# Performance work log

Measured on AMD Instinct MI355X. Metric: run time of the kernel, lower is better.

## Reference

```python
import jax, jax.numpy as jnp
import numpy as np

B, F, N = 16, 64, 32768
C0, C1, C2 = 64, 16, 1
TOP_K = 64
EPS = 1e-5


def setup_inputs() -> dict:
    key = jax.random.key(0)
    ks = jax.random.split(key, 6)
    def rn(k, shape, scale=1.0):
        return jax.random.normal(k, shape, dtype=jnp.float32) * scale
    return {
        "sortvec": rn(ks[0], (B, 1, F, N)),
        "input": rn(ks[1], (B, F, N)),
        # conv0: kernel (F,1), in=1, out=64 -> weight reduces to [C0, F]
        "w0": rn(ks[2], (C0, F), np.sqrt(2.0 / F)), "b0": jnp.zeros((C0,), jnp.float32),
        "w1": rn(ks[3], (C1, C0), np.sqrt(2.0 / C0)), "b1": jnp.zeros((C1,), jnp.float32),
        "w2": rn(ks[4], (C2, C1), np.sqrt(2.0 / C1)), "b2": jnp.zeros((C2,), jnp.float32),
        "g0": jnp.ones((C0,), jnp.float32), "bt0": jnp.zeros((C0,), jnp.float32),
        "g1": jnp.ones((C1,), jnp.float32), "bt1": jnp.zeros((C1,), jnp.float32),
        "g2": jnp.ones((C2,), jnp.float32), "bt2": jnp.zeros((C2,), jnp.float32),
    }


def _bn_relu(x, g, b):
    # training-mode BatchNorm2d over (B, N) per channel; x: [B, C, N]
    mu = jnp.mean(x, axis=(0, 2), keepdims=True)
    var = jnp.var(x, axis=(0, 2), keepdims=True)
    return jax.nn.relu((x - mu) * jax.lax.rsqrt(var + EPS) * g[None, :, None] + b[None, :, None])


def reference(sortvec, input, w0, b0, w1, b1, w2, b2, g0, bt0, g1, bt1, g2, bt2):
    # conv0 with kernel (F,1) collapses the feature axis: [B,1,F,N] -> [B,C0,N]
    x = jnp.einsum('bfn,of->bon', sortvec[:, 0], w0) + b0[None, :, None]
    x = _bn_relu(x, g0, bt0)
    x = _bn_relu(jnp.einsum('bcn,oc->bon', x, w1) + b1[None, :, None], g1, bt1)
    score = _bn_relu(jnp.einsum('bcn,oc->bon', x, w2) + b2[None, :, None], g2, bt2)  # [B,1,N]
    _, idx = jax.lax.top_k(score[:, 0], TOP_K)                                        # [B,K]
    sorted_input = jnp.take_along_axis(input, idx[:, None, :], axis=2)                # [B,F,K]
    sorted_score = jnp.take_along_axis(score, idx[:, None, :], axis=2)                # [B,1,K]
    feat = jnp.concatenate([sorted_input, sorted_score], axis=1)                      # [B,F+1,K]
    return feat, idx
```

## Files before the change

kernel.cpp:

```cpp
#include <hip/hip_runtime.h>


constexpr int   B_   = 16;
constexpr int   N_   = 32768;
constexpr int   K_   = 64;
constexpr long long S_ = (long long)B_ * N_;
constexpr float EPS_ = 1e-5f;

constexpr int NB0   = 2048;
constexpr int NB1   = 2048;
constexpr int NB2   = 256;
constexpr int NBINS = 4096;
constexpr int CAP   = 1024;

__device__ __forceinline__ unsigned key_map(float f) {
  unsigned u = __float_as_uint(f);
  return (u & 0x80000000u) ? ~u : (u | 0x80000000u);
}

__device__ __forceinline__ void gload16(const float* g, float* l) {
  __builtin_amdgcn_global_load_lds(
      (const __attribute__((address_space(1))) void*)g,
      (__attribute__((address_space(3))) void*)l, 16, 0, 0);
}

__device__ __forceinline__ void stage_tile(const float* __restrict__ src,
                                           float (*dst)[64], int t) {
#pragma unroll
  for (int q = 0; q < 4; ++q) {
    const int e = t + q * 256;
    const int f = e >> 4, c4 = (e & 15) << 2;
    gload16(src + (long long)f * N_ + c4, &dst[f][c4]);
  }
}

__global__ __launch_bounds__(256) void k_prep(const float* __restrict__ w0,
                                              const float* __restrict__ w1,
                                              float* __restrict__ w0T,
                                              float* __restrict__ w1p) {
  int t = threadIdx.x;
  for (int e = t; e < 64 * 64; e += 256) {
    int o = e >> 6, f = e & 63;
    w0T[f * 64 + o] = w0[e];
  }
  for (int e = t; e < 16 * 64; e += 256) {
    int cg = e >> 8, rem = e & 255, o = rem >> 4, j = rem & 15;
    w1p[e] = w1[o * 64 + cg * 16 + j];
  }
}

__global__ __launch_bounds__(256) void k_stat0(const float* __restrict__ sv,
                                               const float* __restrict__ w0T,
                                               const float* __restrict__ b0,
                                               float* __restrict__ p0,
                                               int* __restrict__ ghist) {
  __shared__ float svt[2][64][64];
  const int t   = threadIdx.x;
  const int p   = t & 63;
  const int cg  = __builtin_amdgcn_readfirstlane(t >> 6);
  const int bid = blockIdx.x;

  if (t < 32) ghist[bid * 32 + t] = 0;

  float bb[16];
#pragma unroll
  for (int j = 0; j < 16; ++j) bb[j] = b0[cg * 16 + j];

  float s1[16], s2[16];
#pragma unroll
  for (int j = 0; j < 16; ++j) { s1[j] = 0.f; s2[j] = 0.f; }

  {
    const int tile = bid;
    const int b = tile >> 9, n0 = (tile & 511) << 6;
    stage_tile(sv + ((long long)b * 64) * N_ + n0, svt[0], t);
  }
  int cur = 0;
#pragma unroll
  for (int i = 0; i < 4; ++i) {
    __syncthreads();
    if (i + 1 < 4) {
      const int tile = bid + (i + 1) * NB0;
      const int b = tile >> 9, n0 = (tile & 511) << 6;
      stage_tile(sv + ((long long)b * 64) * N_ + n0, svt[cur ^ 1], t);
    }
    float y[16];
#pragma unroll
    for (int j = 0; j < 16; ++j) y[j] = bb[j];
    for (int f = 0; f < 64; ++f) {
      const float x = svt[cur][f][p];
      const float* wr = w0T + f * 64 + cg * 16;
#pragma unroll
      for (int j = 0; j < 16; ++j) y[j] = fmaf(wr[j], x, y[j]);
    }
#pragma unroll
    for (int j = 0; j < 16; ++j) {
      s1[j] += y[j];
      s2[j] = fmaf(y[j], y[j], s2[j]);
    }
    cur ^= 1;
  }

#pragma unroll
  for (int j = 0; j < 16; ++j) {
#pragma unroll
    for (int off = 32; off; off >>= 1) {
      s1[j] += __shfl_down(s1[j], off, 64);
      s2[j] += __shfl_down(s2[j], off, 64);
    }
  }
  if (p == 0) {
    float* dst = p0 + (long long)bid * 128;
#pragma unroll
    for (int j = 0; j < 16; ++j) {
      dst[cg * 16 + j]      = s1[j];
      dst[64 + cg * 16 + j] = s2[j];
    }
  }
}

__global__ __launch_bounds__(1024) void k_reduce0(const float* __restrict__ p0,
                                                  const float* __restrict__ g,
                                                  const float* __restrict__ bt,
                                                  float* __restrict__ st) {
  __shared__ float l[8][128];
  const int t = threadIdx.x;
  const int j = t & 127, grp = t >> 7;
  float a = 0.f;
  for (int i = grp; i < NB0; i += 8) a += p0[(long long)i * 128 + j];
  l[grp][j] = a;
  __syncthreads();
  if (t < 128) {
    float v = ((l[0][t] + l[1][t]) + (l[2][t] + l[3][t])) +
              ((l[4][t] + l[5][t]) + (l[6][t] + l[7][t]));
    l[0][t] = v;
  }
  __syncthreads();
  if (t < 64) {
    const float inv = 1.f / (float)S_;
    float mean = l[0][t] * inv;
    float ex2  = l[0][64 + t] * inv;
    float var  = ex2 - mean * mean;
    float sc   = g[t] * rsqrtf(var + EPS_);
    st[t]      = sc;
    st[64 + t] = bt[t] - mean * sc;
  }
}

__global__ __launch_bounds__(256) void k_layer01(const float* __restrict__ sv,
                                                 const float* __restrict__ w0T,
                                                 const float* __restrict__ b0,
                                                 const float* __restrict__ st0,
                                                 const float* __restrict__ w1p,
                                                 const float* __restrict__ b1,
                                                 float* __restrict__ y1,
                                                 float* __restrict__ p1) {
  __shared__ float svt[2][64][64];
  __shared__ float zp[4][16][64];
  const int t   = threadIdx.x;
  const int p   = t & 63;
  const int cg  = __builtin_amdgcn_readfirstlane(t >> 6);
  const int bid = blockIdx.x;

  float bb[16], sc[16], sh[16];
#pragma unroll
  for (int j = 0; j < 16; ++j) {
    bb[j] = b0[cg * 16 + j];
    sc[j] = st0[cg * 16 + j];
    sh[j] = st0[64 + cg * 16 + j];
  }
  float bb1[4];
#pragma unroll
  for (int j = 0; j < 4; ++j) bb1[j] = b1[cg * 4 + j];

  float sA[4], qA[4];
#pragma unroll
  for (int j = 0; j < 4; ++j) { sA[j] = 0.f; qA[j] = 0.f; }

  {
    const int tile = bid;
    const int b = tile >> 9, n0 = (tile & 511) << 6;
    stage_tile(sv + ((long long)b * 64) * N_ + n0, svt[0], t);
  }
  int cur = 0;
#pragma unroll
  for (int i = 0; i < 4; ++i) {
    const int tile = bid + i * NB0;
    const int b = tile >> 9, n0 = (tile & 511) << 6;

    __syncthreads();
    if (i + 1 < 4) {
      const int tile2 = bid + (i + 1) * NB0;
      const int b2 = tile2 >> 9, n02 = (tile2 & 511) << 6;
      stage_tile(sv + ((long long)b2 * 64) * N_ + n02, svt[cur ^ 1], t);
    }

    float y[16];
#pragma unroll
    for (int j = 0; j < 16; ++j) y[j] = bb[j];
    for (int f = 0; f < 64; ++f) {
      const float x = svt[cur][f][p];
      const float* wr = w0T + f * 64 + cg * 16;
#pragma unroll
      for (int j = 0; j < 16; ++j) y[j] = fmaf(wr[j], x, y[j]);
    }
#pragma unroll
    for (int j = 0; j < 16; ++j) {
      float h = fmaf(y[j], sc[j], sh[j]);
      y[j] = h > 0.f ? h : 0.f;
    }
    const float* wp = w1p + cg * 256;
#pragma unroll
    for (int o = 0; o < 16; ++o) {
      float acc = 0.f;
#pragma unroll
      for (int j = 0; j < 16; ++j) acc = fmaf(wp[o * 16 + j], y[j], acc);
      zp[cg][o][p] = acc;
    }
    __syncthreads();

    float* yo = y1 + ((long long)(b * 16 + cg * 4)) * N_ + n0 + p;
#pragma unroll
    for (int oi = 0; oi < 4; ++oi) {
      const int o = cg * 4 + oi;
      float z = ((zp[0][o][p] + zp[1][o][p]) +
                 (zp[2][o][p] + zp[3][o][p])) + bb1[oi];
      yo[(long long)oi * N_] = z;
      sA[oi] += z;
      qA[oi] = fmaf(z, z, qA[oi]);
    }
    cur ^= 1;
  }

#pragma unroll
  for (int j = 0; j < 4; ++j) {
#pragma unroll
    for (int off = 32; off; off >>= 1) {
      sA[j] += __shfl_down(sA[j], off, 64);
      qA[j] += __shfl_down(qA[j], off, 64);
    }
  }
  if (p == 0) {
    float* dst = p1 + (long long)bid * 32;
#pragma unroll
    for (int j = 0; j < 4; ++j) {
      dst[cg * 4 + j]      = sA[j];
      dst[16 + cg * 4 + j] = qA[j];
    }
  }
}

__global__ __launch_bounds__(1024) void k_reduce1(const float* __restrict__ p1,
                                                  const float* __restrict__ g,
                                                  const float* __restrict__ bt,
                                                  float* __restrict__ st) {
  __shared__ float l[32][32];
  const int t = threadIdx.x;
  const int j = t & 31, grp = t >> 5;
  float a = 0.f;
  for (int i = grp; i < NB1; i += 32) a += p1[(long long)i * 32 + j];
  l[grp][j] = a;
  __syncthreads();
  if (t < 32) {
    float v = 0.f;
#pragma unroll
    for (int g2 = 0; g2 < 32; ++g2) v += l[g2][t];
    l[0][t] = v;
  }
  __syncthreads();
  if (t < 16) {
    const float inv = 1.f / (float)S_;
    float mean = l[0][t] * inv;
    float ex2  = l[0][16 + t] * inv;
    float var  = ex2 - mean * mean;
    float sc   = g[t] * rsqrtf(var + EPS_);
    st[t]      = sc;
    st[16 + t] = bt[t] - mean * sc;
  }
}

__global__ __launch_bounds__(1024) void k_layer2(const float* __restrict__ y1,
                                                 const float* __restrict__ st1,
                                                 const float* __restrict__ w2,
                                                 const float* __restrict__ b2,
                                                 float* __restrict__ y2,
                                                 float* __restrict__ p2,
                                                 int* __restrict__ ghist) {
  __shared__ int hist[NBINS];
  __shared__ float ls[16], lq[16];
  const int t   = threadIdx.x;
  const int blk = blockIdx.x;
  const int b   = blk >> 4;
  const int n0  = ((blk & 15) << 11) | (t << 1);

#pragma unroll
  for (int i = 0; i < NBINS / 1024; ++i) hist[t + i * 1024] = 0;

  float sc[16], sh[16], w[16];
#pragma unroll
  for (int c = 0; c < 16; ++c) { sc[c] = st1[c]; sh[c] = st1[16 + c]; w[c] = w2[c]; }
  const float bias = b2[0];

  float a0 = bias, a1 = bias;
  const float* base = y1 + ((long long)b * 16) * N_ + n0;
#pragma unroll
  for (int c = 0; c < 16; ++c) {
    float2 v = *(const float2*)(base + (long long)c * N_);
    float h;
    h = fmaf(v.x, sc[c], sh[c]); h = h > 0.f ? h : 0.f; a0 = fmaf(w[c], h, a0);
    h = fmaf(v.y, sc[c], sh[c]); h = h > 0.f ? h : 0.f; a1 = fmaf(w[c], h, a1);
  }
  float2 o; o.x = a0; o.y = a1;
  *(float2*)(y2 + (long long)b * N_ + n0) = o;

  __syncthreads();

  atomicAdd(&hist[key_map(a0) >> 20], 1);
  atomicAdd(&hist[key_map(a1) >> 20], 1);

  float ss = a0 + a1;
  float sq = fmaf(a0, a0, a1 * a1);
#pragma unroll
  for (int off = 32; off; off >>= 1) {
    ss += __shfl_down(ss, off, 64);
    sq += __shfl_down(sq, off, 64);
  }
  const int wid = t >> 6, lid = t & 63;
  if (lid == 0) { ls[wid] = ss; lq[wid] = sq; }
  __syncthreads();
  if (t == 0) {
    float Sv = 0.f, Qv = 0.f;
#pragma unroll
    for (int i = 0; i < 16; ++i) { Sv += ls[i]; Qv += lq[i]; }
    p2[blk * 2 + 0] = Sv;
    p2[blk * 2 + 1] = Qv;
  }
#pragma unroll
  for (int i = 0; i < NBINS / 1024; ++i) {
    int v = hist[t + i * 1024];
    if (v) atomicAdd(&ghist[b * NBINS + t + i * 1024], v);
  }
}

__global__ __launch_bounds__(1024) void k_select(const float* __restrict__ y2,
                                                 const int* __restrict__ ghist,
                                                 const float* __restrict__ p2,
                                                 const float* __restrict__ g2,
                                                 const float* __restrict__ bt2,
                                                 const float* __restrict__ inp,
                                                 float* __restrict__ out) {
  __shared__ int hl[NBINS + NBINS / 64];
  __shared__ float sred[512];
  __shared__ unsigned long long cand[CAP];
  __shared__ int lcnt;
  __shared__ int sT;
  __shared__ float s2v[2];
  __shared__ int   idxs[K_];
  __shared__ float scores[K_];

  const int t = threadIdx.x, b = blockIdx.x;
  const int* h = ghist + b * NBINS;
  for (int i = t; i < NBINS; i += 1024) hl[i + (i >> 6)] = h[i];
  if (t < 512) sred[t] = p2[t];
  if (t == 0) lcnt = 0;
  __syncthreads();
  for (int s = 256; s >= 2; s >>= 1) {
    if (t < s) sred[t] += sred[t + s];
    __syncthreads();
  }
  if (t == 0) {
    const float inv = 1.f / (float)S_;
    float mean = sred[0] * inv;
    float var  = sred[1] * inv - mean * mean;
    float scv  = g2[0] * rsqrtf(var + EPS_);
    s2v[0] = scv;
    s2v[1] = bt2[0] - mean * scv;
  }
  if (t < 64) {
    const int l = t;
    int s = 0;
    for (int j = 0; j < 64; ++j) s += hl[(l * 64 + j) + l];
    int Sv = s;
#pragma unroll
    for (int off = 1; off < 64; off <<= 1) {
      int v = __shfl_down(Sv, off, 64);
      if (l + off < 64) Sv += v;
    }
    unsigned long long m = __ballot(Sv >= K_);
    const int lstar = 63 - __builtin_clzll(m);
    const int tailS = (lstar < 63) ? __shfl(Sv, lstar + 1, 64) : 0;
    int Tj = hl[(lstar * 64 + l) + lstar];
#pragma unroll
    for (int off = 1; off < 64; off <<= 1) {
      int v = __shfl_down(Tj, off, 64);
      if (l + off < 64) Tj += v;
    }
    const int cge = Tj + tailS;
    unsigned long long m2 = __ballot(cge >= K_);
    const int jstar = 63 - __builtin_clzll(m2);
    if (l == 0) sT = lstar * 64 + jstar;
  }
  __syncthreads();

  const int T = sT;
  const float* yrow = y2 + (long long)b * N_;
  for (int it = 0; it < 8; ++it) {
    const int n0 = (it << 12) | (t << 2);
    float4 v = *(const float4*)(yrow + n0);
#define DO_CAND(comp, off)                                                    \
    {                                                                         \
      unsigned u = key_map(comp);                                             \
      if ((int)(u >> 20) >= T) {                                              \
        int slot = atomicAdd(&lcnt, 1);                                       \
        if (slot < CAP)                                                       \
          cand[slot] = ((unsigned long long)u << 32) |                        \
                       (unsigned)(N_ - 1 - (n0 + off));                       \
      }                                                                       \
    }
    DO_CAND(v.x, 0) DO_CAND(v.y, 1) DO_CAND(v.z, 2) DO_CAND(v.w, 3)
#undef DO_CAND
  }
  __syncthreads();

  if (t < 64) {
    const int l = t;
    int cn = lcnt;
    if (cn > CAP) cn = CAP;
    unsigned long long k[16];
#pragma unroll
    for (int r = 0; r < 16; ++r) {
      int i = l + r * 64;
      k[r] = (i < cn) ? cand[i] : 0ull;
    }
    unsigned long long curk = 0ull;
#pragma unroll
    for (int r = 0; r < 16; ++r) curk = k[r] > curk ? k[r] : curk;

    int myidx = 0;
    unsigned mymap = 0;
    for (int r = 0; r < K_; ++r) {
      unsigned long long m = curk;
#pragma unroll
      for (int off = 32; off; off >>= 1) {
        unsigned long long o = __shfl_xor(m, off, 64);
        m = o > m ? o : m;
      }
      if (r == l) {
        myidx = N_ - 1 - (int)(m & 0xffffffffu);
        mymap = (unsigned)(m >> 32);
      }
      if (curk == m) {
#pragma unroll
        for (int r2 = 0; r2 < 16; ++r2)
          if (k[r2] == m) k[r2] = 0ull;
        unsigned long long c2 = 0ull;
#pragma unroll
        for (int r2 = 0; r2 < 16; ++r2) c2 = k[r2] > c2 ? k[r2] : c2;
        curk = c2;
      }
    }
    unsigned u = mymap;
    u = (u & 0x80000000u) ? (u & 0x7fffffffu) : ~u;
    float v = __uint_as_float(u);
    float scv = fmaf(v, s2v[0], s2v[1]);
    scores[l] = scv > 0.f ? scv : 0.f;
    idxs[l]   = myidx;
  }
  __syncthreads();

  const float* ib = inp + ((long long)b * 64) * N_;
  for (int e = t; e < 65 * 64; e += 1024) {
    const int f = e >> 6, k = e & 63;
    out[((long long)b * 65 + f) * 64 + k] =
        (f < 64) ? ib[(long long)f * N_ + idxs[k]] : scores[k];
  }
  if (t < K_) out[(long long)B_ * 65 * 64 + b * 64 + t] = (float)idxs[t];
}

extern "C" void kernel_launch(void* const* d_in, const int* in_sizes, int n_in,
                              void* d_out, int out_size, void* d_ws, size_t ws_size,
                              hipStream_t stream) {
  const float* sv  = (const float*)d_in[0];
  const float* inp = (const float*)d_in[1];
  const float* w0  = (const float*)d_in[2];
  const float* b0  = (const float*)d_in[3];
  const float* w1  = (const float*)d_in[4];
  const float* b1  = (const float*)d_in[5];
  const float* w2  = (const float*)d_in[6];
  const float* b2  = (const float*)d_in[7];
  const float* g0  = (const float*)d_in[8];
  const float* bt0 = (const float*)d_in[9];
  const float* g1  = (const float*)d_in[10];
  const float* bt1 = (const float*)d_in[11];
  const float* g2  = (const float*)d_in[12];
  const float* bt2 = (const float*)d_in[13];
  float* out = (float*)d_out;

  float* ws  = (float*)d_ws;
  float* y1  = ws;
  float* y2  = y1 + (size_t)S_ * 16;
  float* p0  = y2 + (size_t)S_;
  float* p1  = p0 + (size_t)NB0 * 128;
  float* p2  = p1 + (size_t)NB1 * 32;
  float* st0 = p2 + 512;
  float* st1 = st0 + 128;
  float* w0T = st1 + 32;
  float* w1p = w0T + 4096;
  int*   ghist = (int*)(w1p + 1024);

  k_prep   <<<1,     256, 0, stream>>>(w0, w1, w0T, w1p);
  k_stat0  <<<NB0,   256, 0, stream>>>(sv, w0T, b0, p0, ghist);
  k_reduce0<<<1,    1024, 0, stream>>>(p0, g0, bt0, st0);
  k_layer01<<<NB1,   256, 0, stream>>>(sv, w0T, b0, st0, w1p, b1, y1, p1);
  k_reduce1<<<1,    1024, 0, stream>>>(p1, g1, bt1, st1);
  k_layer2 <<<NB2,  1024, 0, stream>>>(y1, st1, w2, b2, y2, p2, ghist);
  k_select <<<B_,   1024, 0, stream>>>(y2, ghist, p2, g2, bt2, inp, out);
}
```

Baseline: 291.1 us.

## Fuse layer0/layer1 stages into cooperative persistent kernel, materialize conv0 output

```diff
diff --git a/kernel.cpp b/kernel.cpp
--- a/kernel.cpp
+++ b/kernel.cpp
@@ -1,4 +1,7 @@
 #include <hip/hip_runtime.h>
+#include <hip/hip_cooperative_groups.h>
+
+namespace cg = cooperative_groups;
 
 
 constexpr int   B_   = 16;
@@ -7,8 +10,8 @@
 constexpr long long S_ = (long long)B_ * N_;
 constexpr float EPS_ = 1e-5f;
 
-constexpr int NB0   = 2048;
-constexpr int NB1   = 2048;
+constexpr int NT    = 8192;
+constexpr int MAXNB = 1024;
 constexpr int NB2   = 256;
 constexpr int NBINS = 4096;
 constexpr int CAP   = 1024;
@@ -25,76 +28,71 @@
 }
 
 __device__ __forceinline__ void stage_tile(const float* __restrict__ src,
-                                           float (*dst)[64], int t) {
+                                           float* __restrict__ dst, int t) {
 #pragma unroll
   for (int q = 0; q < 4; ++q) {
     const int e = t + q * 256;
     const int f = e >> 4, c4 = (e & 15) << 2;
-    gload16(src + (long long)f * N_ + c4, &dst[f][c4]);
-  }
-}
-
-__global__ __launch_bounds__(256) void k_prep(const float* __restrict__ w0,
-                                              const float* __restrict__ w1,
-                                              float* __restrict__ w0T,
-                                              float* __restrict__ w1p) {
-  int t = threadIdx.x;
-  for (int e = t; e < 64 * 64; e += 256) {
-    int o = e >> 6, f = e & 63;
-    w0T[f * 64 + o] = w0[e];
-  }
-  for (int e = t; e < 16 * 64; e += 256) {
-    int cg = e >> 8, rem = e & 255, o = rem >> 4, j = rem & 15;
-    w1p[e] = w1[o * 64 + cg * 16 + j];
-  }
-}
-
-__global__ __launch_bounds__(256) void k_stat0(const float* __restrict__ sv,
-                                               const float* __restrict__ w0T,
-                                               const float* __restrict__ b0,
-                                               float* __restrict__ p0,
-                                               int* __restrict__ ghist) {
-  __shared__ float svt[2][64][64];
-  const int t   = threadIdx.x;
+    gload16(src + (long long)f * N_ + c4, dst + f * 64 + c4);
+  }
+}
+
+__device__ __forceinline__ void phase_prep(const float* __restrict__ w0,
+                                           const float* __restrict__ w1,
+                                           float* __restrict__ w0T,
+                                           float* __restrict__ w1T, int t) {
+  for (int e = t; e < 4096; e += 256)
+    w0T[(e & 63) * 64 + (e >> 6)] = w0[e];
+  for (int e = t; e < 1024; e += 256) {
+    const int o = e >> 6, c = e & 63;
+    w1T[c * 16 + o] = w1[e];
+  }
+}
+
+__device__ void phase_conv0(const float* __restrict__ sv,
+                            const float* __restrict__ w0T,
+                            const float* __restrict__ b0,
+                            float* __restrict__ y0,
+                            float* __restrict__ p0,
+                            int* __restrict__ ghist,
+                            float* smem, int t, int bid, int nb) {
   const int p   = t & 63;
-  const int cg  = __builtin_amdgcn_readfirstlane(t >> 6);
-  const int bid = blockIdx.x;
-
-  if (t < 32) ghist[bid * 32 + t] = 0;
+  const int cgq = __builtin_amdgcn_readfirstlane(t >> 6);
+
+  for (int e = bid * 256 + t; e < B_ * NBINS; e += nb * 256) ghist[e] = 0;
 
   float bb[16];
 #pragma unroll
-  for (int j = 0; j < 16; ++j) bb[j] = b0[cg * 16 + j];
-
+  for (int j = 0; j < 16; ++j) bb[j] = b0[cgq * 16 + j];
   float s1[16], s2[16];
 #pragma unroll
   for (int j = 0; j < 16; ++j) { s1[j] = 0.f; s2[j] = 0.f; }
 
-  {
-    const int tile = bid;
-    const int b = tile >> 9, n0 = (tile & 511) << 6;
-    stage_tile(sv + ((long long)b * 64) * N_ + n0, svt[0], t);
-  }
+  stage_tile(sv + ((long long)(bid >> 9) * 64) * N_ + ((bid & 511) << 6),
+             smem, t);
   int cur = 0;
-#pragma unroll
-  for (int i = 0; i < 4; ++i) {
+  for (int tile = bid; tile < NT; tile += nb) {
     __syncthreads();
-    if (i + 1 < 4) {
-      const int tile = bid + (i + 1) * NB0;
-      const int b = tile >> 9, n0 = (tile & 511) << 6;
-      stage_tile(sv + ((long long)b * 64) * N_ + n0, svt[cur ^ 1], t);
-    }
+    const int nxt = tile + nb;
+    if (nxt < NT)
+      stage_tile(sv + ((long long)(nxt >> 9) * 64) * N_ + ((nxt & 511) << 6),
+                 smem + (cur ^ 1) * 4096, t);
+
+    const float* svt = smem + cur * 4096;
     float y[16];
 #pragma unroll
     for (int j = 0; j < 16; ++j) y[j] = bb[j];
     for (int f = 0; f < 64; ++f) {
-      const float x = svt[cur][f][p];
-      const float* wr = w0T + f * 64 + cg * 16;
+      const float x = svt[f * 64 + p];
+      const float* wr = w0T + f * 64 + cgq * 16;
 #pragma unroll
       for (int j = 0; j < 16; ++j) y[j] = fmaf(wr[j], x, y[j]);
     }
+    const int b = tile >> 9, n0 = (tile & 511) << 6;
+    float* dst = y0 + ((long long)(b * 64 + cgq * 16)) * N_ + n0 + p;
 #pragma unroll
     for (int j = 0; j < 16; ++j) {
+      dst[(long long)j * N_] = y[j];
       s1[j] += y[j];
       s2[j] = fmaf(y[j], y[j], s2[j]);
     }
@@ -113,33 +111,28 @@
     float* dst = p0 + (long long)bid * 128;
 #pragma unroll
     for (int j = 0; j < 16; ++j) {
-      dst[cg * 16 + j]      = s1[j];
-      dst[64 + cg * 16 + j] = s2[j];
-    }
-  }
-}
-
-__global__ __launch_bounds__(1024) void k_reduce0(const float* __restrict__ p0,
-                                                  const float* __restrict__ g,
-                                                  const float* __restrict__ bt,
-                                                  float* __restrict__ st) {
-  __shared__ float l[8][128];
-  const int t = threadIdx.x;
+      dst[cgq * 16 + j]      = s1[j];
+      dst[64 + cgq * 16 + j] = s2[j];
+    }
+  }
+}
+
+__device__ void reduce0_dev(const float* __restrict__ p0,
+                            const float* __restrict__ g,
+                            const float* __restrict__ bt,
+                            float* __restrict__ st,
+                            float* l, int t, int nb) {
   const int j = t & 127, grp = t >> 7;
   float a = 0.f;
-  for (int i = grp; i < NB0; i += 8) a += p0[(long long)i * 128 + j];
-  l[grp][j] = a;
-  __syncthreads();
-  if (t < 128) {
-    float v = ((l[0][t] + l[1][t]) + (l[2][t] + l[3][t])) +
-              ((l[4][t] + l[5][t]) + (l[6][t] + l[7][t]));
-    l[0][t] = v;
-  }
+  for (int i = grp; i < nb; i += 2) a += p0[(long long)i * 128 + j];
+  l[grp * 128 + j] = a;
+  __syncthreads();
+  if (t < 128) l[t] = l[t] + l[128 + t];
   __syncthreads();
   if (t < 64) {
     const float inv = 1.f / (float)S_;
-    float mean = l[0][t] * inv;
-    float ex2  = l[0][64 + t] * inv;
+    float mean = l[t] * inv;
+    float ex2  = l[64 + t] * inv;
     float var  = ex2 - mean * mean;
     float sc   = g[t] * rsqrtf(var + EPS_);
     st[t]      = sc;
@@ -147,136 +140,148 @@
   }
 }
 
-__global__ __launch_bounds__(256) void k_layer01(const float* __restrict__ sv,
-                                                 const float* __restrict__ w0T,
-                                                 const float* __restrict__ b0,
-                                                 const float* __restrict__ st0,
-                                                 const float* __restrict__ w1p,
-                                                 const float* __restrict__ b1,
-                                                 float* __restrict__ y1,
-                                                 float* __restrict__ p1) {
-  __shared__ float svt[2][64][64];
-  __shared__ float zp[4][16][64];
-  const int t   = threadIdx.x;
-  const int p   = t & 63;
-  const int cg  = __builtin_amdgcn_readfirstlane(t >> 6);
-  const int bid = blockIdx.x;
-
-  float bb[16], sc[16], sh[16];
+__device__ void phase_bn1(const float* __restrict__ y0,
+                          const float* __restrict__ st0,
+                          const float* __restrict__ w1T,
+                          const float* __restrict__ b1,
+                          float* __restrict__ y1,
+                          float* __restrict__ p1,
+                          float* smem, int t, int bid, int nb) {
+  float s1[16], s2[16];
+#pragma unroll
+  for (int j = 0; j < 16; ++j) { s1[j] = 0.f; s2[j] = 0.f; }
+
+  const long long stride = (long long)nb * 256;
+  for (long long pos = (long long)bid * 256 + t; pos < S_; pos += stride) {
+    const int b = (int)(pos >> 15);
+    const int n = (int)(pos & (N_ - 1));
+    const float* xp = y0 + ((long long)b * 64) * N_ + n;
+
+    float z[16];
+#pragma unroll
+    for (int j = 0; j < 16; ++j) z[j] = b1[j];
+#pragma unroll 8
+    for (int c = 0; c < 64; ++c) {
+      float v = xp[(long long)c * N_];
+      float h = fmaf(v, st0[c], st0[64 + c]);
+      h = h > 0.f ? h : 0.f;
+      const float* wr = w1T + c * 16;
+#pragma unroll
+      for (int j = 0; j < 16; ++j) z[j] = fmaf(wr[j], h, z[j]);
+    }
+    float* yo = y1 + ((long long)b * 16) * N_ + n;
+#pragma unroll
+    for (int j = 0; j < 16; ++j) {
+      yo[(long long)j * N_] = z[j];
+      s1[j] += z[j];
+      s2[j] = fmaf(z[j], z[j], s2[j]);
+    }
+  }
+
+  const int wid = t >> 6, lid = t & 63;
 #pragma unroll
   for (int j = 0; j < 16; ++j) {
-    bb[j] = b0[cg * 16 + j];
-    sc[j] = st0[cg * 16 + j];
-    sh[j] = st0[64 + cg * 16 + j];
-  }
-  float bb1[4];
-#pragma unroll
-  for (int j = 0; j < 4; ++j) bb1[j] = b1[cg * 4 + j];
-
-  float sA[4], qA[4];
-#pragma unroll
-  for (int j = 0; j < 4; ++j) { sA[j] = 0.f; qA[j] = 0.f; }
-
-  {
-    const int tile = bid;
-    const int b = tile >> 9, n0 = (tile & 511) << 6;
-    stage_tile(sv + ((long long)b * 64) * N_ + n0, svt[0], t);
-  }
-  int cur = 0;
-#pragma unroll
-  for (int i = 0; i < 4; ++i) {
-    const int tile = bid + i * NB0;
-    const int b = tile >> 9, n0 = (tile & 511) << 6;
-
-    __syncthreads();
-    if (i + 1 < 4) {
-      const int tile2 = bid + (i + 1) * NB0;
-      const int b2 = tile2 >> 9, n02 = (tile2 & 511) << 6;
-      stage_tile(sv + ((long long)b2 * 64) * N_ + n02, svt[cur ^ 1], t);
-    }
-
-    float y[16];
-#pragma unroll
-    for (int j = 0; j < 16; ++j) y[j] = bb[j];
-    for (int f = 0; f < 64; ++f) {
-      const float x = svt[cur][f][p];
-      const float* wr = w0T + f * 64 + cg * 16;
-#pragma unroll
-      for (int j = 0; j < 16; ++j) y[j] = fmaf(wr[j], x, y[j]);
-    }
-#pragma unroll
-    for (int j = 0; j < 16; ++j) {
-      float h = fmaf(y[j], sc[j], sh[j]);
-      y[j] = h > 0.f ? h : 0.f;
-    }
-    const float* wp = w1p + cg * 256;
-#pragma unroll
-    for (int o = 0; o < 16; ++o) {
-      float acc = 0.f;
-#pragma unroll
-      for (int j = 0; j < 16; ++j) acc = fmaf(wp[o * 16 + j], y[j], acc);
-      zp[cg][o][p] = acc;
-    }
-    __syncthreads();
-
-    float* yo = y1 + ((long long)(b * 16 + cg * 4)) * N_ + n0 + p;
-#pragma unroll
-    for (int oi = 0; oi < 4; ++oi) {
-      const int o = cg * 4 + oi;
-      float z = ((zp[0][o][p] + zp[1][o][p]) +
-                 (zp[2][o][p] + zp[3][o][p])) + bb1[oi];
-      yo[(long long)oi * N_] = z;
-      sA[oi] += z;
-      qA[oi] = fmaf(z, z, qA[oi]);
-    }
-    cur ^= 1;
-  }
-
-#pragma unroll
-  for (int j = 0; j < 4; ++j) {
+    float a = s1[j], q = s2[j];
 #pragma unroll
     for (int off = 32; off; off >>= 1) {
-      sA[j] += __shfl_down(sA[j], off, 64);
-      qA[j] += __shfl_down(qA[j], off, 64);
-    }
-  }
-  if (p == 0) {
-    float* dst = p1 + (long long)bid * 32;
-#pragma unroll
-    for (int j = 0; j < 4; ++j) {
-      dst[cg * 4 + j]      = sA[j];
-      dst[16 + cg * 4 + j] = qA[j];
-    }
-  }
-}
-
-__global__ __launch_bounds__(1024) void k_reduce1(const float* __restrict__ p1,
-                                                  const float* __restrict__ g,
-                                                  const float* __restrict__ bt,
-                                                  float* __restrict__ st) {
-  __shared__ float l[32][32];
-  const int t = threadIdx.x;
+      a += __shfl_down(a, off, 64);
+      q += __shfl_down(q, off, 64);
+    }
+    if (lid == 0) { smem[wid * 32 + j] = a; smem[wid * 32 + 16 + j] = q; }
+  }
+  __syncthreads();
+  if (t < 32)
+    p1[(long long)bid * 32 + t] =
+        (smem[t] + smem[32 + t]) + (smem[64 + t] + smem[96 + t]);
+}
+
+__device__ void reduce1_dev(const float* __restrict__ p1,
+                            const float* __restrict__ g,
+                            const float* __restrict__ bt,
+                            float* __restrict__ st,
+                            float* l, int t, int nb) {
   const int j = t & 31, grp = t >> 5;
   float a = 0.f;
-  for (int i = grp; i < NB1; i += 32) a += p1[(long long)i * 32 + j];
-  l[grp][j] = a;
+  for (int i = grp; i < nb; i += 8) a += p1[(long long)i * 32 + j];
+  l[grp * 32 + j] = a;
   __syncthreads();
   if (t < 32) {
     float v = 0.f;
 #pragma unroll
-    for (int g2 = 0; g2 < 32; ++g2) v += l[g2][t];
-    l[0][t] = v;
+    for (int g2 = 0; g2 < 8; ++g2) v += l[g2 * 32 + t];
+    l[t] = v;
   }
   __syncthreads();
   if (t < 16) {
     const float inv = 1.f / (float)S_;
-    float mean = l[0][t] * inv;
-    float ex2  = l[0][16 + t] * inv;
+    float mean = l[t] * inv;
+    float ex2  = l[16 + t] * inv;
     float var  = ex2 - mean * mean;
     float sc   = g[t] * rsqrtf(var + EPS_);
     st[t]      = sc;
     st[16 + t] = bt[t] - mean * sc;
   }
+}
+
+__global__ __launch_bounds__(256, 4) void k_fused(
+    const float* __restrict__ sv, const float* __restrict__ w0,
+    const float* __restrict__ b0, const float* __restrict__ w1,
+    const float* __restrict__ b1, const float* __restrict__ g0,
+    const float* __restrict__ bt0, const float* __restrict__ g1,
+    const float* __restrict__ bt1, float* __restrict__ w0T,
+    float* __restrict__ w1T, float* __restrict__ st0,
+    float* __restrict__ st1, float* __restrict__ p0,
+    float* __restrict__ p1, float* __restrict__ y0,
+    float* __restrict__ y1, int* __restrict__ ghist) {
+  __shared__ float smem[8192];
+  const int t = threadIdx.x, bid = blockIdx.x, nb = gridDim.x;
+  cg::grid_group grid = cg::this_grid();
+
+  if (bid == 0) phase_prep(w0, w1, w0T, w1T, t);
+  __threadfence();
+  grid.sync();
+
+  phase_conv0(sv, w0T, b0, y0, p0, ghist, smem, t, bid, nb);
+  __threadfence();
+  grid.sync();
+
+  if (bid == 0) reduce0_dev(p0, g0, bt0, st0, smem, t, nb);
+  __threadfence();
+  grid.sync();
+
+  phase_bn1(y0, st0, w1T, b1, y1, p1, smem, t, bid, nb);
+  __threadfence();
+  grid.sync();
+
+  if (bid == 0) reduce1_dev(p1, g1, bt1, st1, smem, t, nb);
+}
+
+__global__ __launch_bounds__(256) void k_prep_w(const float* w0, const float* w1,
+                                                float* w0T, float* w1T) {
+  phase_prep(w0, w1, w0T, w1T, threadIdx.x);
+}
+__global__ __launch_bounds__(256, 4) void k_phA(const float* sv, const float* w0T,
+                                                const float* b0, float* y0,
+                                                float* p0, int* ghist) {
+  __shared__ float smem[8192];
+  phase_conv0(sv, w0T, b0, y0, p0, ghist, smem, threadIdx.x, blockIdx.x,
+              gridDim.x);
+}
+__global__ __launch_bounds__(256) void k_red0w(const float* p0, const float* g,
+                                               const float* bt, float* st, int nb) {
+  __shared__ float l[256];
+  reduce0_dev(p0, g, bt, st, l, threadIdx.x, nb);
+}
+__global__ __launch_bounds__(256, 4) void k_phB(const float* y0, const float* st0,
+                                                const float* w1T, const float* b1,
+                                                float* y1, float* p1) {
+  __shared__ float smem[128];
+  phase_bn1(y0, st0, w1T, b1, y1, p1, smem, threadIdx.x, blockIdx.x, gridDim.x);
+}
+__global__ __launch_bounds__(256) void k_red1w(const float* p1, const float* g,
+                                               const float* bt, float* st, int nb) {
+  __shared__ float l[256];
+  reduce1_dev(p1, g, bt, st, l, threadIdx.x, nb);
 }
 
 __global__ __launch_bounds__(1024) void k_layer2(const float* __restrict__ y1,
@@ -497,22 +502,48 @@
   float* out = (float*)d_out;
 
   float* ws  = (float*)d_ws;
-  float* y1  = ws;
+  float* y0  = ws;
+  float* y1  = y0 + (size_t)S_ * 64;
   float* y2  = y1 + (size_t)S_ * 16;
   float* p0  = y2 + (size_t)S_;
-  float* p1  = p0 + (size_t)NB0 * 128;
-  float* p2  = p1 + (size_t)NB1 * 32;
+  float* p1  = p0 + (size_t)MAXNB * 128;
+  float* p2  = p1 + (size_t)MAXNB * 32;
   float* st0 = p2 + 512;
   float* st1 = st0 + 128;
   float* w0T = st1 + 32;
-  float* w1p = w0T + 4096;
-  int*   ghist = (int*)(w1p + 1024);
-
-  k_prep   <<<1,     256, 0, stream>>>(w0, w1, w0T, w1p);
-  k_stat0  <<<NB0,   256, 0, stream>>>(sv, w0T, b0, p0, ghist);
-  k_reduce0<<<1,    1024, 0, stream>>>(p0, g0, bt0, st0);
-  k_layer01<<<NB1,   256, 0, stream>>>(sv, w0T, b0, st0, w1p, b1, y1, p1);
-  k_reduce1<<<1,    1024, 0, stream>>>(p1, g1, bt1, st1);
-  k_layer2 <<<NB2,  1024, 0, stream>>>(y1, st1, w2, b2, y2, p2, ghist);
-  k_select <<<B_,   1024, 0, stream>>>(y2, ghist, p2, g2, bt2, inp, out);
-}
+  float* w1T = w0T + 4096;
+  int*   ghist = (int*)(w1T + 1024);
+
+  int dev = 0, coop = 0, ncu = 0, maxb = 0;
+  hipGetDevice(&dev);
+  hipDeviceGetAttribute(&coop, hipDeviceAttributeCooperativeLaunch, dev);
+  hipDeviceGetAttribute(&ncu, hipDeviceAttributeMultiprocessorCount, dev);
+  hipOccupancyMaxActiveBlocksPerMultiprocessor(&maxb, (const void*)k_fused,
+                                               256, 0);
+
+  bool fused_done = false;
+  if (coop && ncu > 0 && maxb > 0) {
+    int grid = ncu * maxb;
+    if (grid > MAXNB) grid = MAXNB;
+    if (grid >= 64) {
+      void* args[] = {(void*)&sv,  (void*)&w0,  (void*)&b0,  (void*)&w1,
+                      (void*)&b1,  (void*)&g0,  (void*)&bt0, (void*)&g1,
+                      (void*)&bt1, (void*)&w0T, (void*)&w1T, (void*)&st0,
+                      (void*)&st1, (void*)&p0,  (void*)&p1,  (void*)&y0,
+                      (void*)&y1,  (void*)&ghist};
+      if (hipLaunchCooperativeKernel((void*)k_fused, dim3(grid), dim3(256),
+                                     args, 0, stream) == hipSuccess)
+        fused_done = true;
+    }
+  }
+  if (!fused_done) {
+    k_prep_w<<<1,     256, 0, stream>>>(w0, w1, w0T, w1T);
+    k_phA   <<<MAXNB, 256, 0, stream>>>(sv, w0T, b0, y0, p0, ghist);
+    k_red0w <<<1,     256, 0, stream>>>(p0, g0, bt0, st0, MAXNB);
+    k_phB   <<<MAXNB, 256, 0, stream>>>(y0, st0, w1T, b1, y1, p1);
+    k_red1w <<<1,     256, 0, stream>>>(p1, g1, bt1, st1, MAXNB);
+  }
+
+  k_layer2<<<NB2, 1024, 0, stream>>>(y1, st1, w2, b2, y2, p2, ghist);
+  k_select<<<B_,  1024, 0, stream>>>(y2, ghist, p2, g2, bt2, inp, out);
+}
```

After: 988.5 us. 3.4x slower.
